# Kernel tuning notes

Measured on AMD Instinct MI355X. Metric: run time of the kernel, lower is better.

The kernel has to match this reference:

```python
import jax, jax.numpy as jnp
import numpy as np
from jax import lax

B, NM, P, F, E, H, K = 32, 131072, 256, 3, 64, 4, 3
DH = E // H


def layer_norm(x, gamma, beta, eps=1e-5):
    mu = x.mean(-1, keepdims=True)
    var = ((x - mu) ** 2).mean(-1, keepdims=True)
    return (x - mu) * lax.rsqrt(var + eps) * gamma + beta


def knn_interp(x, pos_x, pos_y, k=K):
    """x: [B, Nx, F] features at pos_x [Nx, 2]; interpolate to pos_y [Ny, 2].
    Positions are shared across the batch (they are tiled in the torch code),
    so KNN indices/weights are computed once. Matches torch knn + inverse-
    squared-distance weighted scatter (uniform per-batch counts => gather form).
    """
    d2 = jnp.sum((pos_y[:, None, :] - pos_x[None, :, :]) ** 2, axis=-1)  # [Ny, Nx]
    neg_d2, idx = lax.top_k(-d2, k)                                      # [Ny, k]
    w = 1.0 / jnp.clip(-neg_d2, 1e-16)                                   # [Ny, k]
    w = lax.stop_gradient(w)  # torch computes weights under no_grad
    gathered = x[:, idx, :]                                              # [B, Ny, k, F]
    num = jnp.sum(gathered * w[None, :, :, None], axis=2)                # [B, Ny, F]
    den = jnp.sum(w, axis=1)[None, :, None]                              # [1, Ny, 1]
    return num / den


def setup_inputs() -> dict:
    key = jax.random.key(0)
    ks = jax.random.split(key, 8)
    return {
        "node_attr": jax.random.normal(ks[0], (B * NM, F), jnp.float32),
        "position_mesh": jax.random.uniform(ks[1], (NM, 2), jnp.float32),
        "position_pivotal": jax.random.uniform(ks[2], (P, 2), jnp.float32),
        "ln_gamma": jnp.ones((F,), jnp.float32),
        "ln_beta": jnp.zeros((F,), jnp.float32),
        "Wf": jax.random.normal(ks[3], (E, F), jnp.float32) * (2.0 / E) ** 0.5,
        "bf": jnp.zeros((E,), jnp.float32),
        "Wp": jax.random.normal(ks[4], (E, 2), jnp.float32) * (2.0 / E) ** 0.5,
        "bp": jnp.zeros((E,), jnp.float32),
        "in_proj_w": jax.random.normal(ks[5], (3 * E, E), jnp.float32) * (1.0 / E) ** 0.5,
        "in_proj_b": jnp.zeros((3 * E,), jnp.float32),
        "batch_size": B,
    }


def reference(node_attr, position_mesh, position_pivotal, ln_gamma, ln_beta,
              Wf, bf, Wp, bp, in_proj_w, in_proj_b, batch_size):
    x = node_attr.reshape(batch_size, -1, F)                 # [B, NM, F]
    # PivotalNorm after encoder (encoder/decoder MeshGraphNet omitted: undefined dep)
    x = layer_norm(x, ln_gamma, ln_beta)
    # ---- downsample: mesh -> pivotal via inverse-distance KNN interpolation ----
    y = knn_interp(x, position_mesh, position_pivotal)       # [B, P, F]
    # attention-based pooling over pivotal nodes
    q = (jnp.einsum('bpf,ef->bpe', y, Wf) + bf
         + (position_pivotal @ Wp.T + bp)[None])             # [B, P, E]
    Wq, Wk = in_proj_w[:E], in_proj_w[E:2 * E]
    bq, bk = in_proj_b[:E], in_proj_b[E:2 * E]
    Q = (q @ Wq.T + bq).reshape(batch_size, P, H, DH)
    Kt = (q @ Wk.T + bk).reshape(batch_size, P, H, DH)
    scores = jnp.einsum('bqhd,bkhd->bhqk', Q, Kt) / np.float32(np.sqrt(DH))
    attn = jax.nn.softmax(scores, axis=-1)                   # [B, H, P, P]
    attn_w = attn.mean(axis=1)                               # avg heads, [B, P, P]
    y = jnp.einsum('bqk,bkf->bqf', attn_w, y)                # [B, P, F]
    # ---- interpolate: pivotal -> mesh ----
    out = knn_interp(y, position_pivotal, position_mesh)     # [B, NM, F]
    return out.reshape(-1, F)
```

## Files before the change

### kernel.cpp

```cpp
#include <hip/hip_runtime.h>
#include <math.h>

#define NM 131072
#define PP 256
#define BB 32

#define CHUNKS 512
#define CHUNK_SZ 256

#define INF_F 3.0e38f
#define LDW 13

__device__ __forceinline__ void ins3(float d, int i,
    float& d0, float& d1, float& d2, int& i0, int& i1, int& i2) {
  bool l0 = d < d0, l1 = d < d1, l2 = d < d2;
  d2 = l1 ? d1 : (l2 ? d : d2);
  i2 = l1 ? i1 : (l2 ? i : i2);
  d1 = l0 ? d0 : (l1 ? d : d1);
  i1 = l0 ? i0 : (l1 ? i : i1);
  d0 = l0 ? d : d0;
  i0 = l0 ? i : i0;
}

__device__ __forceinline__ float dist2(float ax, float ay, float bx, float by) {
  float dx = ax - bx, dy = ay - by;
  return __fadd_rn(__fmul_rn(dx, dx), __fmul_rn(dy, dy));
}

__global__ __launch_bounds__(1024)
void knnA_partial(const float* __restrict__ mesh, const float* __restrict__ piv,
                  float* __restrict__ candd, int* __restrict__ candi) {
  const int c = blockIdx.x;
  const int tid = threadIdx.x;
  const int p = tid & 255;
  const int sub = tid >> 8;
  __shared__ float sdf[256 * LDW];
  __shared__ int   sif[256 * LDW];

  const float2 pv = ((const float2*)piv)[p];
  float d0 = INF_F, d1 = INF_F, d2 = INF_F;
  int i0 = 0, i1 = 0, i2 = 0;
  const int base = c * CHUNK_SZ + sub * 64;
#pragma unroll 4
  for (int i = 0; i < 64; ++i) {
    float mx = mesh[2 * (base + i)];
    float my = mesh[2 * (base + i) + 1];
    ins3(dist2(pv.x, pv.y, mx, my), base + i, d0, d1, d2, i0, i1, i2);
  }
  sdf[p * LDW + sub * 3 + 0] = d0; sif[p * LDW + sub * 3 + 0] = i0;
  sdf[p * LDW + sub * 3 + 1] = d1; sif[p * LDW + sub * 3 + 1] = i1;
  sdf[p * LDW + sub * 3 + 2] = d2; sif[p * LDW + sub * 3 + 2] = i2;
  __syncthreads();

  if (tid < 256) {
    float e0 = sdf[tid * LDW + 0], e1 = sdf[tid * LDW + 1], e2 = sdf[tid * LDW + 2];
    int j0 = sif[tid * LDW + 0], j1 = sif[tid * LDW + 1], j2 = sif[tid * LDW + 2];
#pragma unroll
    for (int s = 1; s < 4; ++s)
#pragma unroll
      for (int k = 0; k < 3; ++k)
        ins3(sdf[tid * LDW + s * 3 + k], sif[tid * LDW + s * 3 + k], e0, e1, e2, j0, j1, j2);
    int o = (tid * CHUNKS + c) * 3;
    candd[o] = e0; candd[o + 1] = e1; candd[o + 2] = e2;
    candi[o] = j0; candi[o + 1] = j1; candi[o + 2] = j2;
  }
}

__global__ void knnA_merge(const float* __restrict__ candd, const int* __restrict__ candi,
                           float* __restrict__ wA, int* __restrict__ idxA) {
  const int p = blockIdx.x;
  const int t = threadIdx.x;
  __shared__ float sd[PP * 3];
  __shared__ int si[PP * 3];
  __shared__ float sd2[32 * 3];
  __shared__ int si2[32 * 3];

  float d0 = INF_F, d1 = INF_F, d2 = INF_F;
  int i0 = 0, i1 = 0, i2 = 0;
#pragma unroll
  for (int cc = 0; cc < 2; ++cc) {
    int o = (p * CHUNKS + 2 * t + cc) * 3;
#pragma unroll
    for (int k = 0; k < 3; ++k) ins3(candd[o + k], candi[o + k], d0, d1, d2, i0, i1, i2);
  }
  sd[t * 3] = d0; sd[t * 3 + 1] = d1; sd[t * 3 + 2] = d2;
  si[t * 3] = i0; si[t * 3 + 1] = i1; si[t * 3 + 2] = i2;
  __syncthreads();
  if (t < 32) {
    d0 = d1 = d2 = INF_F; i0 = i1 = i2 = 0;
    for (int j = t * 8; j < t * 8 + 8; ++j)
      for (int k = 0; k < 3; ++k) ins3(sd[j * 3 + k], si[j * 3 + k], d0, d1, d2, i0, i1, i2);
    sd2[t * 3] = d0; sd2[t * 3 + 1] = d1; sd2[t * 3 + 2] = d2;
    si2[t * 3] = i0; si2[t * 3 + 1] = i1; si2[t * 3 + 2] = i2;
  }
  __syncthreads();
  if (t == 0) {
    d0 = d1 = d2 = INF_F; i0 = i1 = i2 = 0;
    for (int j = 0; j < 32; ++j)
      for (int k = 0; k < 3; ++k) ins3(sd2[j * 3 + k], si2[j * 3 + k], d0, d1, d2, i0, i1, i2);
    wA[p * 3 + 0] = 1.0f / fmaxf(d0, 1e-16f); idxA[p * 3 + 0] = i0;
    wA[p * 3 + 1] = 1.0f / fmaxf(d1, 1e-16f); idxA[p * 3 + 1] = i1;
    wA[p * 3 + 2] = 1.0f / fmaxf(d2, 1e-16f); idxA[p * 3 + 2] = i2;
  }
}

__global__ void gather_ln(const float* __restrict__ node, const float* __restrict__ wA,
                          const int* __restrict__ idxA, const float* __restrict__ gamma,
                          const float* __restrict__ beta, float* __restrict__ y) {
  const int b = blockIdx.x >> 2;
  const int p = ((blockIdx.x & 3) << 6) + threadIdx.x;
  const float g0 = gamma[0], g1 = gamma[1], g2 = gamma[2];
  const float be0 = beta[0], be1 = beta[1], be2 = beta[2];
  float num0 = 0.f, num1 = 0.f, num2 = 0.f, den = 0.f;
#pragma unroll
  for (int k = 0; k < 3; ++k) {
    int idx = idxA[p * 3 + k];
    float w = wA[p * 3 + k];
    const float* r = node + ((size_t)b * NM + idx) * 3;
    float a0 = r[0], a1 = r[1], a2 = r[2];
    float mu = (a0 + a1 + a2) * (1.0f / 3.0f);
    float e0 = a0 - mu, e1 = a1 - mu, e2 = a2 - mu;
    float var = (e0 * e0 + e1 * e1 + e2 * e2) * (1.0f / 3.0f);
    float sc = 1.0f / sqrtf(var + 1e-5f);
    float v0 = e0 * sc * g0 + be0, v1 = e1 * sc * g1 + be1, v2 = e2 * sc * g2 + be2;
    num0 += v0 * w; num1 += v1 * w; num2 += v2 * w; den += w;
  }
  int o = (b * PP + p) * 3;
  y[o] = num0 / den; y[o + 1] = num1 / den; y[o + 2] = num2 / den;
}

__global__ __launch_bounds__(128, 2)
void qqk_kernel(const float* __restrict__ y, const float* __restrict__ piv,
                const float* __restrict__ Wf, const float* __restrict__ bf,
                const float* __restrict__ Wp, const float* __restrict__ bp,
                const float* __restrict__ ipw, const float* __restrict__ ipb,
                float* __restrict__ Qh, float* __restrict__ Kh) {
  const int b = blockIdx.x >> 5;
  const int ptile = (blockIdx.x & 31) * 8;
  const int t = threadIdx.x;
  const int e = t & 63;
  const int half = t >> 6;
  __shared__ float qs[8][64];

  {
    float wf0 = Wf[e * 3], wf1 = Wf[e * 3 + 1], wf2 = Wf[e * 3 + 2];
    float wp0 = Wp[e * 2], wp1 = Wp[e * 2 + 1];
    float cst = bf[e] + bp[e];
    for (int r = half; r < 8; r += 2) {
      int p = ptile + r;
      const float* yr = y + (b * PP + p) * 3;
      float pe = piv[2 * p] * wp0 + piv[2 * p + 1] * wp1;
      qs[r][e] = yr[0] * wf0 + yr[1] * wf1 + yr[2] * wf2 + cst + pe;
    }
  }
  __syncthreads();

  const int row = half * 64 + e;
  float wreg[64];
  const float4* W4 = (const float4*)(ipw + row * 64);
#pragma unroll
  for (int j = 0; j < 16; ++j) {
    float4 v = W4[j];
    wreg[4 * j] = v.x; wreg[4 * j + 1] = v.y; wreg[4 * j + 2] = v.z; wreg[4 * j + 3] = v.w;
  }
  float bias = ipb[row];
  float* dst = half ? Kh : Qh;
  const int h = e >> 4, d = e & 15;
  for (int r = 0; r < 8; ++r) {
    float acc = bias;
#pragma unroll
    for (int j = 0; j < 64; ++j) acc += qs[r][j] * wreg[j];
    int p = ptile + r;
    dst[(((b * 4 + h) * PP) + p) * 16 + d] = acc;
  }
}

__global__ void attn_kernel(const float* __restrict__ Qh, const float* __restrict__ Kh,
                            const float* __restrict__ y, float* __restrict__ y2) {
  const int b = blockIdx.x >> 3;
  const int h = (blockIdx.x >> 1) & 3;
  const int qh = blockIdx.x & 1;
  const int t = threadIdx.x;
  const int q = qh * 128 + t;

  __shared__ float Ks[PP * 16];
  __shared__ float ys[PP * 3];

  {
    const float4* src = (const float4*)(Kh + (size_t)(b * 4 + h) * PP * 16);
    float4* dst = (float4*)Ks;
#pragma unroll
    for (int j = 0; j < 8; ++j) dst[j * 128 + t] = src[j * 128 + t];
    const float* ysrc = y + b * PP * 3;
#pragma unroll
    for (int j = 0; j < 6; ++j) ys[j * 128 + t] = ysrc[j * 128 + t];
  }
  __syncthreads();

  const float4* q4 = (const float4*)(Qh + ((size_t)((b * 4 + h) * PP) + q) * 16);
  float4 qa = q4[0], qb = q4[1], qc = q4[2], qd = q4[3];

  float m = -INF_F, l = 0.f, a0 = 0.f, a1 = 0.f, a2 = 0.f;
#pragma unroll 4
  for (int k = 0; k < PP; ++k) {
    const float4* kr = (const float4*)(Ks + k * 16);
    float4 k0 = kr[0], k1 = kr[1], k2 = kr[2], k3 = kr[3];
    float dot = qa.x * k0.x + qa.y * k0.y + qa.z * k0.z + qa.w * k0.w
              + qb.x * k1.x + qb.y * k1.y + qb.z * k1.z + qb.w * k1.w
              + qc.x * k2.x + qc.y * k2.y + qc.z * k2.z + qc.w * k2.w
              + qd.x * k3.x + qd.y * k3.y + qd.z * k3.z + qd.w * k3.w;
    float s = dot * 0.25f;
    float mn = fmaxf(m, s);
    float p = __expf(s - mn);
    float sc = __expf(m - mn);
    float y0 = ys[k * 3], y1 = ys[k * 3 + 1], yy2 = ys[k * 3 + 2];
    l = l * sc + p;
    a0 = a0 * sc + p * y0;
    a1 = a1 * sc + p * y1;
    a2 = a2 * sc + p * yy2;
    m = mn;
  }
  float inv = 0.25f / l;
  float* o = y2 + (b * PP + q) * 3;
  atomicAdd(o + 0, a0 * inv);
  atomicAdd(o + 1, a1 * inv);
  atomicAdd(o + 2, a2 * inv);
}

__global__ __launch_bounds__(256)
void knnB_out(const float* __restrict__ mesh, const float* __restrict__ piv,
              const float* __restrict__ y2, float* __restrict__ out) {
  const int tid = threadIdx.x;
  const int ml = tid & 63;
  const int sub = tid >> 6;
  const int m = blockIdx.x * 64 + ml;
  __shared__ float sdf[64 * LDW];
  __shared__ int   sif[64 * LDW];

  const float2 mv = ((const float2*)mesh)[m];
  float d0 = INF_F, d1 = INF_F, d2 = INF_F;
  int i0 = 0, i1 = 0, i2 = 0;
  const int base = sub * 64;
#pragma unroll 4
  for (int i = 0; i < 64; ++i) {
    int idx = base + i;
    float px = piv[2 * idx], py = piv[2 * idx + 1];
    ins3(dist2(mv.x, mv.y, px, py), idx, d0, d1, d2, i0, i1, i2);
  }
  sdf[ml * LDW + sub * 3 + 0] = d0; sif[ml * LDW + sub * 3 + 0] = i0;
  sdf[ml * LDW + sub * 3 + 1] = d1; sif[ml * LDW + sub * 3 + 1] = i1;
  sdf[ml * LDW + sub * 3 + 2] = d2; sif[ml * LDW + sub * 3 + 2] = i2;
  __syncthreads();

  float e0 = sdf[ml * LDW + 0], e1 = sdf[ml * LDW + 1], e2 = sdf[ml * LDW + 2];
  int j0 = sif[ml * LDW + 0], j1 = sif[ml * LDW + 1], j2 = sif[ml * LDW + 2];
#pragma unroll
  for (int s = 1; s < 4; ++s)
#pragma unroll
    for (int k = 0; k < 3; ++k)
      ins3(sdf[ml * LDW + s * 3 + k], sif[ml * LDW + s * 3 + k], e0, e1, e2, j0, j1, j2);

  float w0 = 1.0f / fmaxf(e0, 1e-16f);
  float w1 = 1.0f / fmaxf(e1, 1e-16f);
  float w2 = 1.0f / fmaxf(e2, 1e-16f);
  float inv = 1.0f / (w0 + w1 + w2);
  const int o0 = j0 * 3, o1 = j1 * 3, o2 = j2 * 3;

#pragma unroll 2
  for (int bi = 0; bi < 8; ++bi) {
    const int b = sub * 8 + bi;
    const float* yb = y2 + b * PP * 3;
    float3 r0 = *(const float3*)(yb + o0);
    float3 r1 = *(const float3*)(yb + o1);
    float3 r2 = *(const float3*)(yb + o2);
    float3 res;
    res.x = (w0 * r0.x + w1 * r1.x + w2 * r2.x) * inv;
    res.y = (w0 * r0.y + w1 * r1.y + w2 * r2.y) * inv;
    res.z = (w0 * r0.z + w1 * r1.z + w2 * r2.z) * inv;
    *(float3*)(out + ((size_t)b * NM + m) * 3) = res;
  }
}

extern "C" void kernel_launch(void* const* d_in, const int* in_sizes, int n_in,
                              void* d_out, int out_size, void* d_ws, size_t ws_size,
                              hipStream_t stream) {
  const float* node  = (const float*)d_in[0];
  const float* mesh  = (const float*)d_in[1];
  const float* piv   = (const float*)d_in[2];
  const float* gamma = (const float*)d_in[3];
  const float* beta  = (const float*)d_in[4];
  const float* Wf    = (const float*)d_in[5];
  const float* bf    = (const float*)d_in[6];
  const float* Wp    = (const float*)d_in[7];
  const float* bp    = (const float*)d_in[8];
  const float* ipw   = (const float*)d_in[9];
  const float* ipb   = (const float*)d_in[10];
  float* out = (float*)d_out;

  float* candd = (float*)d_ws;
  int*   candi = (int*)(candd + CHUNKS * PP * 3);
  float* wA    = (float*)(candi + CHUNKS * PP * 3);
  int*   idxA  = (int*)(wA + PP * 3);
  float* y     = (float*)(idxA + PP * 3);
  float* Qh    = y + BB * PP * 3;
  float* Kh    = Qh + BB * PP * 64;
  float* y2    = Kh + BB * PP * 64;

  hipMemsetAsync(y2, 0, BB * PP * 3 * sizeof(float), stream);

  knnA_partial<<<CHUNKS, 1024, 0, stream>>>(mesh, piv, candd, candi);
  knnA_merge<<<PP, 256, 0, stream>>>(candd, candi, wA, idxA);
  gather_ln<<<BB * 4, 64, 0, stream>>>(node, wA, idxA, gamma, beta, y);
  qqk_kernel<<<BB * 32, 128, 0, stream>>>(y, piv, Wf, bf, Wp, bp, ipw, ipb, Qh, Kh);
  attn_kernel<<<BB * 4 * 2, 128, 0, stream>>>(Qh, Kh, y, y2);
  knnB_out<<<NM / 64, 256, 0, stream>>>(mesh, piv, y2, out);
}
```

Measured before the change: 213.2 us.

## Fuse both KNN searches and y2 zeroing into one launch; fuse gather into QK

Mesh-to-pivotal and pivotal-to-mesh KNN searches now run in a single kernel, split by block index, with one extra block that zeroes y2 in place of the memset. Pivotal KNN now uses one block per pivotal point with a tree reduction and a tie-breaking insert. This removes the separate merge kernel and the candidate buffers. The gather plus layer-norm step is folded into the QK projection kernel, and the output kernel only reads precomputed weights and indices. This cuts launch count and removes the KNN work from the output pass, at the cost of an extra buffer of NM×3 weights and indices being written and read back.

```diff
diff --git a/kernel.cpp b/kernel.cpp
--- a/kernel.cpp
+++ b/kernel.cpp
@@ -5,11 +5,11 @@
 #define PP 256
 #define BB 32
 
-#define CHUNKS 512
-#define CHUNK_SZ 256
-
 #define INF_F 3.0e38f
 #define LDW 13
+
+#define KA_BLOCKS 256
+#define KB_BLOCKS 512
 
 __device__ __forceinline__ void ins3(float d, int i,
     float& d0, float& d1, float& d2, int& i0, int& i1, int& i2) {
@@ -22,135 +22,184 @@
   i0 = l0 ? i : i0;
 }
 
+__device__ __forceinline__ bool lt2(float d, int i, float D, int I) {
+  return (d < D) || (d == D && i < I);
+}
+
+__device__ __forceinline__ void ins3t(float d, int i,
+    float& d0, float& d1, float& d2, int& i0, int& i1, int& i2) {
+  bool l0 = lt2(d, i, d0, i0), l1 = lt2(d, i, d1, i1), l2 = lt2(d, i, d2, i2);
+  d2 = l1 ? d1 : (l2 ? d : d2);
+  i2 = l1 ? i1 : (l2 ? i : i2);
+  d1 = l0 ? d0 : (l1 ? d : d1);
+  i1 = l0 ? i0 : (l1 ? i : i1);
+  d0 = l0 ? d : d0;
+  i0 = l0 ? i : i0;
+}
+
 __device__ __forceinline__ float dist2(float ax, float ay, float bx, float by) {
   float dx = ax - bx, dy = ay - by;
   return __fadd_rn(__fmul_rn(dx, dx), __fmul_rn(dy, dy));
 }
 
 __global__ __launch_bounds__(1024)
-void knnA_partial(const float* __restrict__ mesh, const float* __restrict__ piv,
-                  float* __restrict__ candd, int* __restrict__ candi) {
-  const int c = blockIdx.x;
+void fused_knn(const float* __restrict__ mesh, const float* __restrict__ piv,
+               float* __restrict__ wA, int* __restrict__ idxA,
+               float* __restrict__ wB, int* __restrict__ idxB,
+               float* __restrict__ y2) {
+  const int blk = blockIdx.x;
   const int tid = threadIdx.x;
-  const int p = tid & 255;
-  const int sub = tid >> 8;
-  __shared__ float sdf[256 * LDW];
-  __shared__ int   sif[256 * LDW];
-
-  const float2 pv = ((const float2*)piv)[p];
-  float d0 = INF_F, d1 = INF_F, d2 = INF_F;
-  int i0 = 0, i1 = 0, i2 = 0;
-  const int base = c * CHUNK_SZ + sub * 64;
+  __shared__ float sdf[PP * LDW];
+  __shared__ int   sif[PP * LDW];
+
+  if (blk < KA_BLOCKS) {
+    const int p = blk;
+    const float2 pv = ((const float2*)piv)[p];
+    const float2* m2 = (const float2*)mesh;
+    float d0 = INF_F, d1 = INF_F, d2 = INF_F;
+    int i0 = 0, i1 = 0, i2 = 0;
 #pragma unroll 4
-  for (int i = 0; i < 64; ++i) {
-    float mx = mesh[2 * (base + i)];
-    float my = mesh[2 * (base + i) + 1];
-    ins3(dist2(pv.x, pv.y, mx, my), base + i, d0, d1, d2, i0, i1, i2);
-  }
-  sdf[p * LDW + sub * 3 + 0] = d0; sif[p * LDW + sub * 3 + 0] = i0;
-  sdf[p * LDW + sub * 3 + 1] = d1; sif[p * LDW + sub * 3 + 1] = i1;
-  sdf[p * LDW + sub * 3 + 2] = d2; sif[p * LDW + sub * 3 + 2] = i2;
-  __syncthreads();
-
-  if (tid < 256) {
-    float e0 = sdf[tid * LDW + 0], e1 = sdf[tid * LDW + 1], e2 = sdf[tid * LDW + 2];
-    int j0 = sif[tid * LDW + 0], j1 = sif[tid * LDW + 1], j2 = sif[tid * LDW + 2];
-#pragma unroll
-    for (int s = 1; s < 4; ++s)
-#pragma unroll
-      for (int k = 0; k < 3; ++k)
-        ins3(sdf[tid * LDW + s * 3 + k], sif[tid * LDW + s * 3 + k], e0, e1, e2, j0, j1, j2);
-    int o = (tid * CHUNKS + c) * 3;
-    candd[o] = e0; candd[o + 1] = e1; candd[o + 2] = e2;
-    candi[o] = j0; candi[o + 1] = j1; candi[o + 2] = j2;
-  }
-}
-
-__global__ void knnA_merge(const float* __restrict__ candd, const int* __restrict__ candi,
-                           float* __restrict__ wA, int* __restrict__ idxA) {
-  const int p = blockIdx.x;
-  const int t = threadIdx.x;
-  __shared__ float sd[PP * 3];
-  __shared__ int si[PP * 3];
-  __shared__ float sd2[32 * 3];
-  __shared__ int si2[32 * 3];
-
-  float d0 = INF_F, d1 = INF_F, d2 = INF_F;
-  int i0 = 0, i1 = 0, i2 = 0;
-#pragma unroll
-  for (int cc = 0; cc < 2; ++cc) {
-    int o = (p * CHUNKS + 2 * t + cc) * 3;
-#pragma unroll
-    for (int k = 0; k < 3; ++k) ins3(candd[o + k], candi[o + k], d0, d1, d2, i0, i1, i2);
-  }
-  sd[t * 3] = d0; sd[t * 3 + 1] = d1; sd[t * 3 + 2] = d2;
-  si[t * 3] = i0; si[t * 3 + 1] = i1; si[t * 3 + 2] = i2;
-  __syncthreads();
-  if (t < 32) {
-    d0 = d1 = d2 = INF_F; i0 = i1 = i2 = 0;
-    for (int j = t * 8; j < t * 8 + 8; ++j)
-      for (int k = 0; k < 3; ++k) ins3(sd[j * 3 + k], si[j * 3 + k], d0, d1, d2, i0, i1, i2);
-    sd2[t * 3] = d0; sd2[t * 3 + 1] = d1; sd2[t * 3 + 2] = d2;
-    si2[t * 3] = i0; si2[t * 3 + 1] = i1; si2[t * 3 + 2] = i2;
-  }
-  __syncthreads();
-  if (t == 0) {
-    d0 = d1 = d2 = INF_F; i0 = i1 = i2 = 0;
-    for (int j = 0; j < 32; ++j)
-      for (int k = 0; k < 3; ++k) ins3(sd2[j * 3 + k], si2[j * 3 + k], d0, d1, d2, i0, i1, i2);
-    wA[p * 3 + 0] = 1.0f / fmaxf(d0, 1e-16f); idxA[p * 3 + 0] = i0;
-    wA[p * 3 + 1] = 1.0f / fmaxf(d1, 1e-16f); idxA[p * 3 + 1] = i1;
-    wA[p * 3 + 2] = 1.0f / fmaxf(d2, 1e-16f); idxA[p * 3 + 2] = i2;
-  }
-}
-
-__global__ void gather_ln(const float* __restrict__ node, const float* __restrict__ wA,
-                          const int* __restrict__ idxA, const float* __restrict__ gamma,
-                          const float* __restrict__ beta, float* __restrict__ y) {
-  const int b = blockIdx.x >> 2;
-  const int p = ((blockIdx.x & 3) << 6) + threadIdx.x;
-  const float g0 = gamma[0], g1 = gamma[1], g2 = gamma[2];
-  const float be0 = beta[0], be1 = beta[1], be2 = beta[2];
-  float num0 = 0.f, num1 = 0.f, num2 = 0.f, den = 0.f;
-#pragma unroll
-  for (int k = 0; k < 3; ++k) {
-    int idx = idxA[p * 3 + k];
-    float w = wA[p * 3 + k];
-    const float* r = node + ((size_t)b * NM + idx) * 3;
-    float a0 = r[0], a1 = r[1], a2 = r[2];
-    float mu = (a0 + a1 + a2) * (1.0f / 3.0f);
-    float e0 = a0 - mu, e1 = a1 - mu, e2 = a2 - mu;
-    float var = (e0 * e0 + e1 * e1 + e2 * e2) * (1.0f / 3.0f);
-    float sc = 1.0f / sqrtf(var + 1e-5f);
-    float v0 = e0 * sc * g0 + be0, v1 = e1 * sc * g1 + be1, v2 = e2 * sc * g2 + be2;
-    num0 += v0 * w; num1 += v1 * w; num2 += v2 * w; den += w;
-  }
-  int o = (b * PP + p) * 3;
-  y[o] = num0 / den; y[o + 1] = num1 / den; y[o + 2] = num2 / den;
+    for (int j = 0; j < 128; ++j) {
+      int idx = tid + (j << 10);
+      float2 mp = m2[idx];
+      ins3(dist2(pv.x, pv.y, mp.x, mp.y), idx, d0, d1, d2, i0, i1, i2);
+    }
+    sdf[tid * 3 + 0] = d0; sif[tid * 3 + 0] = i0;
+    sdf[tid * 3 + 1] = d1; sif[tid * 3 + 1] = i1;
+    sdf[tid * 3 + 2] = d2; sif[tid * 3 + 2] = i2;
+    __syncthreads();
+
+    if (tid < 128) {
+      float e0 = INF_F, e1 = INF_F, e2 = INF_F; int j0 = 0, j1 = 0, j2 = 0;
+#pragma unroll
+      for (int s = 0; s < 8; ++s) {
+        int o = (tid + 128 * s) * 3;
+#pragma unroll
+        for (int k = 0; k < 3; ++k) ins3t(sdf[o + k], sif[o + k], e0, e1, e2, j0, j1, j2);
+      }
+      sdf[tid * 3 + 0] = e0; sif[tid * 3 + 0] = j0;
+      sdf[tid * 3 + 1] = e1; sif[tid * 3 + 1] = j1;
+      sdf[tid * 3 + 2] = e2; sif[tid * 3 + 2] = j2;
+    }
+    __syncthreads();
+
+    if (tid < 16) {
+      float e0 = INF_F, e1 = INF_F, e2 = INF_F; int j0 = 0, j1 = 0, j2 = 0;
+#pragma unroll
+      for (int s = 0; s < 8; ++s) {
+        int o = (tid + 16 * s) * 3;
+#pragma unroll
+        for (int k = 0; k < 3; ++k) ins3t(sdf[o + k], sif[o + k], e0, e1, e2, j0, j1, j2);
+      }
+      sdf[tid * 3 + 0] = e0; sif[tid * 3 + 0] = j0;
+      sdf[tid * 3 + 1] = e1; sif[tid * 3 + 1] = j1;
+      sdf[tid * 3 + 2] = e2; sif[tid * 3 + 2] = j2;
+    }
+    __syncthreads();
+
+    if (tid == 0) {
+      float e0 = INF_F, e1 = INF_F, e2 = INF_F; int j0 = 0, j1 = 0, j2 = 0;
+      for (int s = 0; s < 16; ++s) {
+        int o = s * 3;
+#pragma unroll
+        for (int k = 0; k < 3; ++k) ins3t(sdf[o + k], sif[o + k], e0, e1, e2, j0, j1, j2);
+      }
+      wA[p * 3 + 0] = 1.0f / fmaxf(e0, 1e-16f); idxA[p * 3 + 0] = j0;
+      wA[p * 3 + 1] = 1.0f / fmaxf(e1, 1e-16f); idxA[p * 3 + 1] = j1;
+      wA[p * 3 + 2] = 1.0f / fmaxf(e2, 1e-16f); idxA[p * 3 + 2] = j2;
+    }
+  } else if (blk < KA_BLOCKS + KB_BLOCKS) {
+    const int bi = blk - KA_BLOCKS;
+    const int ml = tid & 255;
+    const int sub = tid >> 8;
+    const int m = bi * 256 + ml;
+    const float2 mv = ((const float2*)mesh)[m];
+    float d0 = INF_F, d1 = INF_F, d2 = INF_F;
+    int i0 = 0, i1 = 0, i2 = 0;
+    const int base = sub * 64;
+#pragma unroll 4
+    for (int i = 0; i < 64; ++i) {
+      int idx = base + i;
+      float px = piv[2 * idx], py = piv[2 * idx + 1];
+      ins3(dist2(mv.x, mv.y, px, py), idx, d0, d1, d2, i0, i1, i2);
+    }
+    sdf[ml * LDW + sub * 3 + 0] = d0; sif[ml * LDW + sub * 3 + 0] = i0;
+    sdf[ml * LDW + sub * 3 + 1] = d1; sif[ml * LDW + sub * 3 + 1] = i1;
+    sdf[ml * LDW + sub * 3 + 2] = d2; sif[ml * LDW + sub * 3 + 2] = i2;
+    __syncthreads();
+
+    if (tid < 256) {
+      float e0 = sdf[tid * LDW + 0], e1 = sdf[tid * LDW + 1], e2 = sdf[tid * LDW + 2];
+      int j0 = sif[tid * LDW + 0], j1 = sif[tid * LDW + 1], j2 = sif[tid * LDW + 2];
+#pragma unroll
+      for (int s = 1; s < 4; ++s)
+#pragma unroll
+        for (int k = 0; k < 3; ++k)
+          ins3(sdf[tid * LDW + s * 3 + k], sif[tid * LDW + s * 3 + k], e0, e1, e2, j0, j1, j2);
+      const int m0 = bi * 256 + tid;
+      wB[m0 * 3 + 0] = 1.0f / fmaxf(e0, 1e-16f); idxB[m0 * 3 + 0] = j0;
+      wB[m0 * 3 + 1] = 1.0f / fmaxf(e1, 1e-16f); idxB[m0 * 3 + 1] = j1;
+      wB[m0 * 3 + 2] = 1.0f / fmaxf(e2, 1e-16f); idxB[m0 * 3 + 2] = j2;
+    }
+  } else {
+    float4 z; z.x = 0.f; z.y = 0.f; z.z = 0.f; z.w = 0.f;
+    float4* p4 = (float4*)y2;
+#pragma unroll
+    for (int j = 0; j < 6; ++j) p4[tid + (j << 10)] = z;
+  }
 }
 
 __global__ __launch_bounds__(128, 2)
-void qqk_kernel(const float* __restrict__ y, const float* __restrict__ piv,
+void gather_qqk(const float* __restrict__ node, const float* __restrict__ piv,
+                const float* __restrict__ gamma, const float* __restrict__ beta,
                 const float* __restrict__ Wf, const float* __restrict__ bf,
                 const float* __restrict__ Wp, const float* __restrict__ bp,
                 const float* __restrict__ ipw, const float* __restrict__ ipb,
-                float* __restrict__ Qh, float* __restrict__ Kh) {
+                const float* __restrict__ wA, const int* __restrict__ idxA,
+                float* __restrict__ y, float* __restrict__ Qh, float* __restrict__ Kh) {
   const int b = blockIdx.x >> 5;
   const int ptile = (blockIdx.x & 31) * 8;
   const int t = threadIdx.x;
+  __shared__ float qs[8][64];
+  __shared__ float ys[8][3];
+
+  if (t < 8) {
+    const int p = ptile + t;
+    const float g0 = gamma[0], g1 = gamma[1], g2 = gamma[2];
+    const float be0 = beta[0], be1 = beta[1], be2 = beta[2];
+    float num0 = 0.f, num1 = 0.f, num2 = 0.f, den = 0.f;
+#pragma unroll
+    for (int k = 0; k < 3; ++k) {
+      int idx = idxA[p * 3 + k];
+      float w = wA[p * 3 + k];
+      const float* r = node + ((size_t)b * NM + idx) * 3;
+      float a0 = r[0], a1 = r[1], a2 = r[2];
+      float mu = (a0 + a1 + a2) * (1.0f / 3.0f);
+      float e0 = a0 - mu, e1 = a1 - mu, e2 = a2 - mu;
+      float var = (e0 * e0 + e1 * e1 + e2 * e2) * (1.0f / 3.0f);
+      float sc = 1.0f / sqrtf(var + 1e-5f);
+      num0 += (e0 * sc * g0 + be0) * w;
+      num1 += (e1 * sc * g1 + be1) * w;
+      num2 += (e2 * sc * g2 + be2) * w;
+      den += w;
+    }
+    float o0 = num0 / den, o1 = num1 / den, o2 = num2 / den;
+    ys[t][0] = o0; ys[t][1] = o1; ys[t][2] = o2;
+    float* yr = y + (b * PP + p) * 3;
+    yr[0] = o0; yr[1] = o1; yr[2] = o2;
+  }
+  __syncthreads();
+
   const int e = t & 63;
   const int half = t >> 6;
-  __shared__ float qs[8][64];
-
   {
     float wf0 = Wf[e * 3], wf1 = Wf[e * 3 + 1], wf2 = Wf[e * 3 + 2];
     float wp0 = Wp[e * 2], wp1 = Wp[e * 2 + 1];
     float cst = bf[e] + bp[e];
     for (int r = half; r < 8; r += 2) {
       int p = ptile + r;
-      const float* yr = y + (b * PP + p) * 3;
       float pe = piv[2 * p] * wp0 + piv[2 * p + 1] * wp1;
-      qs[r][e] = yr[0] * wf0 + yr[1] * wf1 + yr[2] * wf2 + cst + pe;
+      qs[r][e] = ys[r][0] * wf0 + ys[r][1] * wf1 + ys[r][2] * wf2 + cst + pe;
     }
   }
   __syncthreads();
@@ -228,43 +277,16 @@
 }
 
 __global__ __launch_bounds__(256)
-void knnB_out(const float* __restrict__ mesh, const float* __restrict__ piv,
-              const float* __restrict__ y2, float* __restrict__ out) {
+void interp_out(const float* __restrict__ wB, const int* __restrict__ idxB,
+                const float* __restrict__ y2, float* __restrict__ out) {
   const int tid = threadIdx.x;
   const int ml = tid & 63;
   const int sub = tid >> 6;
   const int m = blockIdx.x * 64 + ml;
-  __shared__ float sdf[64 * LDW];
-  __shared__ int   sif[64 * LDW];
-
-  const float2 mv = ((const float2*)mesh)[m];
-  float d0 = INF_F, d1 = INF_F, d2 = INF_F;
-  int i0 = 0, i1 = 0, i2 = 0;
-  const int base = sub * 64;
-#pragma unroll 4
-  for (int i = 0; i < 64; ++i) {
-    int idx = base + i;
-    float px = piv[2 * idx], py = piv[2 * idx + 1];
-    ins3(dist2(mv.x, mv.y, px, py), idx, d0, d1, d2, i0, i1, i2);
-  }
-  sdf[ml * LDW + sub * 3 + 0] = d0; sif[ml * LDW + sub * 3 + 0] = i0;
-  sdf[ml * LDW + sub * 3 + 1] = d1; sif[ml * LDW + sub * 3 + 1] = i1;
-  sdf[ml * LDW + sub * 3 + 2] = d2; sif[ml * LDW + sub * 3 + 2] = i2;
-  __syncthreads();
-
-  float e0 = sdf[ml * LDW + 0], e1 = sdf[ml * LDW + 1], e2 = sdf[ml * LDW + 2];
-  int j0 = sif[ml * LDW + 0], j1 = sif[ml * LDW + 1], j2 = sif[ml * LDW + 2];
-#pragma unroll
-  for (int s = 1; s < 4; ++s)
-#pragma unroll
-    for (int k = 0; k < 3; ++k)
-      ins3(sdf[ml * LDW + s * 3 + k], sif[ml * LDW + s * 3 + k], e0, e1, e2, j0, j1, j2);
-
-  float w0 = 1.0f / fmaxf(e0, 1e-16f);
-  float w1 = 1.0f / fmaxf(e1, 1e-16f);
-  float w2 = 1.0f / fmaxf(e2, 1e-16f);
-  float inv = 1.0f / (w0 + w1 + w2);
-  const int o0 = j0 * 3, o1 = j1 * 3, o2 = j2 * 3;
+
+  const float w0 = wB[m * 3 + 0], w1 = wB[m * 3 + 1], w2 = wB[m * 3 + 2];
+  const int o0 = idxB[m * 3 + 0] * 3, o1 = idxB[m * 3 + 1] * 3, o2 = idxB[m * 3 + 2] * 3;
+  const float inv = 1.0f / (w0 + w1 + w2);
 
 #pragma unroll 2
   for (int bi = 0; bi < 8; ++bi) {
@@ -297,21 +319,18 @@
   const float* ipb   = (const float*)d_in[10];
   float* out = (float*)d_out;
 
-  float* candd = (float*)d_ws;
-  int*   candi = (int*)(candd + CHUNKS * PP * 3);
-  float* wA    = (float*)(candi + CHUNKS * PP * 3);
-  int*   idxA  = (int*)(wA + PP * 3);
-  float* y     = (float*)(idxA + PP * 3);
-  float* Qh    = y + BB * PP * 3;
-  float* Kh    = Qh + BB * PP * 64;
-  float* y2    = Kh + BB * PP * 64;
-
-  hipMemsetAsync(y2, 0, BB * PP * 3 * sizeof(float), stream);
-
-  knnA_partial<<<CHUNKS, 1024, 0, stream>>>(mesh, piv, candd, candi);
-  knnA_merge<<<PP, 256, 0, stream>>>(candd, candi, wA, idxA);
-  gather_ln<<<BB * 4, 64, 0, stream>>>(node, wA, idxA, gamma, beta, y);
-  qqk_kernel<<<BB * 32, 128, 0, stream>>>(y, piv, Wf, bf, Wp, bp, ipw, ipb, Qh, Kh);
+  float* wA   = (float*)d_ws;
+  int*   idxA = (int*)(wA + PP * 3);
+  float* y    = (float*)(idxA + PP * 3);
+  float* Qh   = y + BB * PP * 3;
+  float* Kh   = Qh + BB * PP * 64;
+  float* y2   = Kh + BB * PP * 64;
+  float* wB   = y2 + BB * PP * 3;
+  int*   idxB = (int*)(wB + NM * 3);
+
+  fused_knn<<<KA_BLOCKS + KB_BLOCKS + 1, 1024, 0, stream>>>(mesh, piv, wA, idxA, wB, idxB, y2);
+  gather_qqk<<<BB * 32, 128, 0, stream>>>(node, piv, gamma, beta, Wf, bf, Wp, bp, ipw, ipb,
+                                          wA, idxA, y, Qh, Kh);
   attn_kernel<<<BB * 4 * 2, 128, 0, stream>>>(Qh, Kh, y, y2);
-  knnB_out<<<NM / 64, 256, 0, stream>>>(mesh, piv, y2, out);
-}
+  interp_out<<<NM / 64, 256, 0, stream>>>(wB, idxB, y2, out);
+}
```

New measurement: 199.4 us. -6.5%, faster.
